# Performance work log

Hardware: AMD Instinct MI355X
Metric: run time of the kernel (lower is better)

Reference implementation:

```python
import jax, jax.numpy as jnp
import numpy as np

K = 64  # top-k sparsity level

def setup_inputs() -> dict:
    key = jax.random.key(0)
    x = jax.random.normal(key, (8192, 16384), dtype=jnp.float32)
    return {"x": x}

def reference(x):
    # top-k along last dim, ReLU post-activation, scatter into zeros
    vals, idx = jax.lax.top_k(x, K)                     # [B, K]
    vals = jax.nn.relu(vals)
    rows = jnp.arange(x.shape[0])[:, None]              # [B, 1]
    out = jnp.zeros_like(x).at[rows, idx].set(vals)     # indices are unique per row
    return out
```

## Files before the change

### kernel.cpp

```cpp
#include <hip/hip_runtime.h>
#include <stdint.h>


#define COLS 16384
#define K_SEL 64
#define CAP 4096
#define BLOCK 256

__global__ __launch_bounds__(BLOCK) void topk_relu_scatter(
    const float* __restrict__ x, float* __restrict__ out) {
  __shared__ unsigned long long cand[CAP];
  __shared__ int cnt;

  const int row = blockIdx.x;
  const int tid = threadIdx.x;
  const float* xr = x + (size_t)row * COLS;
  float* orow = out + (size_t)row * COLS;
  const float4* xr4 = (const float4*)xr;

  const float ladder[3] = {2.0f, 1.0f, 0.0f};
  int ncand = 0;
  for (int lv = 0; lv < 3; ++lv) {
    if (tid == 0) cnt = 0;
    __syncthreads();
    const float thr = ladder[lv];
#pragma unroll
    for (int it = 0; it < COLS / 4 / BLOCK; ++it) {
      const int vi = it * BLOCK + tid;
      float4 v = xr4[vi];
      const int base = vi * 4;
      float vv[4] = {v.x, v.y, v.z, v.w};
#pragma unroll
      for (int c = 0; c < 4; ++c) {
        if (vv[c] > thr) {
          int p = atomicAdd(&cnt, 1);
          if (p < CAP) {
            unsigned key = __float_as_uint(vv[c]);
            cand[p] = ((unsigned long long)key << 32) |
                      (unsigned)(~(base + c));
          }
        }
      }
    }
    __syncthreads();
    ncand = cnt;
    if (ncand >= K_SEL || lv == 2) break;
    __syncthreads();
  }

  int m = ncand < CAP ? ncand : CAP;
  int n = 64;
  while (n < m) n <<= 1;
  for (int i = m + tid; i < n; i += BLOCK) cand[i] = 0ULL;
  __syncthreads();

  for (int k2 = 2; k2 <= n; k2 <<= 1) {
    for (int j = k2 >> 1; j > 0; j >>= 1) {
      for (int i = tid; i < n; i += BLOCK) {
        int ixj = i ^ j;
        if (ixj > i) {
          unsigned long long a = cand[i], b = cand[ixj];
          bool up = ((i & k2) == 0);
          if ((a > b) == up) { cand[i] = b; cand[ixj] = a; }
        }
      }
      __syncthreads();
    }
  }

  float4 z = make_float4(0.f, 0.f, 0.f, 0.f);
  float4* o4 = (float4*)orow;
#pragma unroll
  for (int it = 0; it < COLS / 4 / BLOCK; ++it) o4[it * BLOCK + tid] = z;
  __threadfence_block();
  __syncthreads();

  int S = K_SEL < m ? K_SEL : m;
  if (tid < S) {
    unsigned long long c = cand[n - 1 - tid];
    unsigned idx = ~(unsigned)(c & 0xFFFFFFFFULL);
    float val = __uint_as_float((unsigned)(c >> 32));
    orow[idx] = val;
  }
}

extern "C" void kernel_launch(void* const* d_in, const int* in_sizes, int n_in,
                              void* d_out, int out_size, void* d_ws, size_t ws_size,
                              hipStream_t stream) {
  const float* x = (const float*)d_in[0];
  float* out = (float*)d_out;
  const int rows = out_size / COLS;
  topk_relu_scatter<<<dim3(rows), dim3(BLOCK), 0, stream>>>(x, out);
}
```

Baseline: 1.007 ms.

## Cache row in registers, tighten threshold ladder, prune bitonic sort stages

Each thread now loads its 64 floats of the row into registers once and zeroes the output up front, so the threshold passes rescan registers instead of re-reading global memory. The threshold ladder moves to 2.4/2.0/0.0 and the candidate buffer shrinks to 2048, which cuts the number of candidates to sort and the shared memory per block. The bitonic sort skips the low merge stages of the final pass, since only the top 64 are needed, and it only synchronises when a stage compares elements 64 or more apart. Launch bounds request 4 blocks per SM. The risks are high register pressure from the 16 float4 per thread, and syncs being skipped on the assumption that a 64-lane wavefront runs in lockstep, which may not be safe for the strided accesses used here.

```diff
diff --git a/kernel.cpp b/kernel.cpp
--- a/kernel.cpp
+++ b/kernel.cpp
@@ -4,40 +4,46 @@
 
 #define COLS 16384
 #define K_SEL 64
-#define CAP 4096
+#define CAP 2048
 #define BLOCK 256
+#define NV (COLS / 4 / BLOCK)
 
-__global__ __launch_bounds__(BLOCK) void topk_relu_scatter(
+__global__ __launch_bounds__(BLOCK, 4) void topk_relu_scatter(
     const float* __restrict__ x, float* __restrict__ out) {
   __shared__ unsigned long long cand[CAP];
   __shared__ int cnt;
 
   const int row = blockIdx.x;
   const int tid = threadIdx.x;
-  const float* xr = x + (size_t)row * COLS;
+  const float4* xr4 = (const float4*)(x + (size_t)row * COLS);
   float* orow = out + (size_t)row * COLS;
-  const float4* xr4 = (const float4*)xr;
+  float4* o4 = (float4*)orow;
 
-  const float ladder[3] = {2.0f, 1.0f, 0.0f};
+  float4 vbuf[NV];
+  const float4 z = make_float4(0.f, 0.f, 0.f, 0.f);
+#pragma unroll
+  for (int it = 0; it < NV; ++it) {
+    vbuf[it] = xr4[it * BLOCK + tid];
+    o4[it * BLOCK + tid] = z;
+  }
+
   int ncand = 0;
+  const float ladder[3] = {2.4f, 2.0f, 0.0f};
   for (int lv = 0; lv < 3; ++lv) {
     if (tid == 0) cnt = 0;
     __syncthreads();
     const float thr = ladder[lv];
 #pragma unroll
-    for (int it = 0; it < COLS / 4 / BLOCK; ++it) {
-      const int vi = it * BLOCK + tid;
-      float4 v = xr4[vi];
-      const int base = vi * 4;
-      float vv[4] = {v.x, v.y, v.z, v.w};
+    for (int it = 0; it < NV; ++it) {
+      const int base = (it * BLOCK + tid) * 4;
+      float vv[4] = {vbuf[it].x, vbuf[it].y, vbuf[it].z, vbuf[it].w};
 #pragma unroll
       for (int c = 0; c < 4; ++c) {
         if (vv[c] > thr) {
           int p = atomicAdd(&cnt, 1);
           if (p < CAP) {
-            unsigned key = __float_as_uint(vv[c]);
-            cand[p] = ((unsigned long long)key << 32) |
-                      (unsigned)(~(base + c));
+            cand[p] = ((unsigned long long)__float_as_uint(vv[c]) << 32)
+                      | (unsigned)(~(base + c));
           }
         }
       }
@@ -48,39 +54,36 @@
     __syncthreads();
   }
 
-  int m = ncand < CAP ? ncand : CAP;
+  const int m = ncand < CAP ? ncand : CAP;
   int n = 64;
   while (n < m) n <<= 1;
   for (int i = m + tid; i < n; i += BLOCK) cand[i] = 0ULL;
   __syncthreads();
 
+  int prevj = 0;
   for (int k2 = 2; k2 <= n; k2 <<= 1) {
-    for (int j = k2 >> 1; j > 0; j >>= 1) {
+    const int jmin = (k2 == n && n > 64) ? 64 : 1;
+    for (int j = k2 >> 1; j >= jmin; j >>= 1) {
+      if (j >= 64 || prevj >= 64) __syncthreads();
       for (int i = tid; i < n; i += BLOCK) {
-        int ixj = i ^ j;
+        const int ixj = i ^ j;
         if (ixj > i) {
-          unsigned long long a = cand[i], b = cand[ixj];
-          bool up = ((i & k2) == 0);
+          const unsigned long long a = cand[i], b = cand[ixj];
+          const bool up = ((i & k2) == 0);
           if ((a > b) == up) { cand[i] = b; cand[ixj] = a; }
         }
       }
-      __syncthreads();
+      prevj = j;
     }
   }
-
-  float4 z = make_float4(0.f, 0.f, 0.f, 0.f);
-  float4* o4 = (float4*)orow;
-#pragma unroll
-  for (int it = 0; it < COLS / 4 / BLOCK; ++it) o4[it * BLOCK + tid] = z;
   __threadfence_block();
   __syncthreads();
 
-  int S = K_SEL < m ? K_SEL : m;
+  const int S = K_SEL < m ? K_SEL : m;
   if (tid < S) {
-    unsigned long long c = cand[n - 1 - tid];
-    unsigned idx = ~(unsigned)(c & 0xFFFFFFFFULL);
-    float val = __uint_as_float((unsigned)(c >> 32));
-    orow[idx] = val;
+    const unsigned long long c = cand[n - 1 - tid];
+    const unsigned idx = ~(unsigned)(c & 0xFFFFFFFFu);
+    orow[idx] = __uint_as_float((unsigned)(c >> 32));
   }
 }
 
```

Result: faster. 955.0 us (-5.2%).
